# Optimization experiments

Hardware: AMD Instinct MI355X
Metric: run time of the kernel (lower is better)

Reference implementation:

```python
import jax, jax.numpy as jnp
import numpy as np

B, M, D, H = 32, 1024, 768, 256


def setup_inputs() -> dict:
    key = jax.random.key(0)
    k = jax.random.split(key, 6)
    V = jax.random.normal(k[0], (B, M, D), dtype=jnp.float32)
    alpha = jnp.float32(0.5)
    # torch nn.Linear weights: [out, in]
    WV_w = jax.random.normal(k[1], (H, D), dtype=jnp.float32) * (1.0 / np.sqrt(D))
    WV_b = jnp.zeros((H,), dtype=jnp.float32)
    W_conv = jax.random.normal(k[2], (H, H), dtype=jnp.float32) * (1.0 / np.sqrt(H))
    res_w = jax.random.normal(k[3], (H, D), dtype=jnp.float32) * (1.0 / np.sqrt(D))
    res_b = jnp.zeros((H,), dtype=jnp.float32)
    return {"V": V, "alpha": alpha, "WV_w": WV_w, "WV_b": WV_b,
            "W_conv": W_conv, "res_w": res_w, "res_b": res_b}


def reference(V, alpha, WV_w, WV_b, W_conv, res_w, res_b):
    # global feature awareness enhancement: alpha*V + (1-alpha)*mean
    g = jnp.mean(V, axis=1, keepdims=True)            # [B,1,D]
    V_enh = alpha * V + (1.0 - alpha) * g             # [B,M,D]
    # projection (torch Linear: x @ W.T + b)
    Vp = jnp.einsum('bmd,hd->bmh', V_enh, WV_w) + WV_b  # [B,M,H]
    # dynamic incidence matrix: row-softmax of Vp @ Vp.T
    sim = jnp.einsum('bmh,bnh->bmn', Vp, Vp)          # [B,M,M]
    H_TV = jax.nn.softmax(sim, axis=-1)               # [B,M,M]
    # hypergraph convolution: H @ ((H.T @ X) @ W)
    t1 = jnp.einsum('bnm,bnh->bmh', H_TV, Vp)         # H.T @ X -> [B,M,H]
    t2 = jnp.einsum('bmh,hk->bmk', t1, W_conv)        # [B,M,H]
    O = jnp.einsum('bmn,bnh->bmh', H_TV, t2)          # [B,M,H]
    # residual projection + relu
    res = jnp.einsum('bmd,hd->bmh', V, res_w) + res_b  # [B,M,H]
    return jax.nn.relu(O + res)
```

## Files before the change

### kernel.cpp

```cpp
#include <hip/hip_runtime.h>
#include <math.h>


#define PADK 40

typedef __attribute__((ext_vector_type(8))) short bf16x8;
typedef __attribute__((ext_vector_type(4))) float f32x4;

__device__ __forceinline__ ushort f2b(float f) {
    unsigned u = __float_as_uint(f);
    return (ushort)((u + 0x7fffu + ((u >> 16) & 1u)) >> 16);
}
__device__ __forceinline__ float b2f(ushort u) {
    return __uint_as_float((unsigned)u << 16);
}
__device__ __forceinline__ uint4 pack8(float4 a, float4 b) {
    uint4 r;
    r.x = f2b(a.x) | ((unsigned)f2b(a.y) << 16);
    r.y = f2b(a.z) | ((unsigned)f2b(a.w) << 16);
    r.z = f2b(b.x) | ((unsigned)f2b(b.y) << 16);
    r.w = f2b(b.z) | ((unsigned)f2b(b.w) << 16);
    return r;
}

template<bool CASTA>
__device__ __forceinline__ void gemm_core(const void* __restrict__ Av, int lda,
                                          const ushort* __restrict__ Bt, int ldb, int K,
                                          ushort* As, ushort* Bs, f32x4 acc[4][4]) {
    const int tid = threadIdx.x;
    const int lane = tid & 63;
    const int r0 = tid >> 2;
    const int c0 = (tid & 3) * 8;
    const int kg = (lane >> 4) * 8;
    const int rr = lane & 15;
    const int wave = tid >> 6;
    const int wr = (wave >> 1) * 64, wc = (wave & 1) * 64;
    ushort* as0 = As + r0 * PADK + c0;
    ushort* as1 = As + (r0 + 64) * PADK + c0;
    ushort* bs0 = Bs + r0 * PADK + c0;
    ushort* bs1 = Bs + (r0 + 64) * PADK + c0;
    const ushort* bt0 = Bt + (size_t)r0 * ldb + c0;
    const ushort* bt1 = Bt + (size_t)(r0 + 64) * ldb + c0;

    for (int k0 = 0; k0 < K; k0 += 32) {
        uint4 aw0, aw1;
        if constexpr (CASTA) {
            const float* fA = (const float*)Av;
            const float* pa0 = fA + (size_t)r0 * lda + k0 + c0;
            const float* pa1 = fA + (size_t)(r0 + 64) * lda + k0 + c0;
            aw0 = pack8(*(const float4*)pa0, *(const float4*)(pa0 + 4));
            aw1 = pack8(*(const float4*)pa1, *(const float4*)(pa1 + 4));
        } else {
            const ushort* uA = (const ushort*)Av;
            aw0 = *(const uint4*)(uA + (size_t)r0 * lda + k0 + c0);
            aw1 = *(const uint4*)(uA + (size_t)(r0 + 64) * lda + k0 + c0);
        }
        uint4 bw0 = *(const uint4*)(bt0 + k0);
        uint4 bw1 = *(const uint4*)(bt1 + k0);
        __syncthreads();
        *(uint4*)as0 = aw0; *(uint4*)as1 = aw1;
        *(uint4*)bs0 = bw0; *(uint4*)bs1 = bw1;
        __syncthreads();
        bf16x8 av[4], bv[4];
        #pragma unroll
        for (int i = 0; i < 4; ++i) {
            av[i] = *(const bf16x8*)(As + (wr + i * 16 + rr) * PADK + kg);
            bv[i] = *(const bf16x8*)(Bs + (wc + i * 16 + rr) * PADK + kg);
        }
        #pragma unroll
        for (int i = 0; i < 4; ++i)
            #pragma unroll
            for (int j = 0; j < 4; ++j)
                acc[i][j] = __builtin_amdgcn_mfma_f32_16x16x32_bf16(av[i], bv[j], acc[i][j], 0, 0, 0);
    }
}

#define EPI_COORDS \
    const int lane = threadIdx.x & 63; \
    const int wave = threadIdx.x >> 6; \
    const int rb = (wave >> 1) * 64 + (lane >> 4) * 4; \
    const int cb = (wave & 1) * 64 + (lane & 15);

__global__ __launch_bounds__(256) void k_mean(const float* __restrict__ V, float* __restrict__ gpart) {
    const int b = blockIdx.z, mc = blockIdx.y;
    const int d = blockIdx.x * 256 + threadIdx.x;
    const float* Vb = V + ((size_t)(b * 1024 + mc * 128)) * 768 + d;
    float s = 0.f;
    for (int m = 0; m < 128; ++m) s += Vb[(size_t)m * 768];
    gpart[(size_t)(mc * 32 + b) * 768 + d] = s;
}

__global__ __launch_bounds__(256) void k_gsum(const float* __restrict__ gpart, float* __restrict__ g) {
    int idx = blockIdx.x * 256 + threadIdx.x;
    float s = 0.f;
    #pragma unroll
    for (int c = 0; c < 8; ++c) s += gpart[(size_t)c * 24576 + idx];
    g[idx] = s * (1.0f / 1024.0f);
}

__global__ __launch_bounds__(256) void k_gW(const float* __restrict__ g,
                                            const float* __restrict__ WVw,
                                            float* __restrict__ gW) {
    int idx = blockIdx.x * 256 + threadIdx.x;
    int b = idx >> 8, h = idx & 255;
    const float* gr = g + b * 768;
    const float* wr = WVw + (size_t)h * 768;
    float s = 0.f;
    for (int d = 0; d < 768; ++d) s += gr[d] * wr[d];
    gW[idx] = s;
}

__global__ __launch_bounds__(256) void k_castw(const float* __restrict__ WVw,
                                               const float* __restrict__ resw,
                                               ushort* __restrict__ Wcat) {
    int id = blockIdx.x * 256 + threadIdx.x;
    int n = id / 96, c = (id - n * 96) * 8;
    const float* src = (n < 256) ? (WVw + (size_t)n * 768 + c) : (resw + (size_t)(n - 256) * 768 + c);
    *(uint4*)(Wcat + (size_t)n * 768 + c) = pack8(*(const float4*)src, *(const float4*)(src + 4));
}

__global__ __launch_bounds__(256) void k_wct(const float* __restrict__ Wc, ushort* __restrict__ WcT) {
    __shared__ float t[64][65];
    const int r0 = blockIdx.y * 64, c0 = blockIdx.x * 64;
    const int tid = threadIdx.x;
    #pragma unroll
    for (int i = 0; i < 4; ++i) {
        int r = (tid >> 4) + i * 16, c4 = (tid & 15) * 4;
        float4 v = *(const float4*)&Wc[(size_t)(r0 + r) * 256 + c0 + c4];
        t[r][c4] = v.x; t[r][c4 + 1] = v.y; t[r][c4 + 2] = v.z; t[r][c4 + 3] = v.w;
    }
    __syncthreads();
    #pragma unroll
    for (int i = 0; i < 4; ++i) {
        int oc = (tid >> 4) + i * 16, r4 = (tid & 15) * 4;
        unsigned lo = f2b(t[r4][oc]) | ((unsigned)f2b(t[r4 + 1][oc]) << 16);
        unsigned hi = f2b(t[r4 + 2][oc]) | ((unsigned)f2b(t[r4 + 3][oc]) << 16);
        *(uint2*)&WcT[(size_t)(c0 + oc) * 256 + r0 + r4] = make_uint2(lo, hi);
    }
}

__global__ __launch_bounds__(256) void k_trb(const ushort* __restrict__ in, ushort* __restrict__ out,
                                             int R, int C, int ldin) {
    __shared__ ushort t[64][68];
    const int b = blockIdx.z;
    const ushort* ib = in + (size_t)b * R * ldin;
    ushort* ob = out + (size_t)b * R * C;
    const int c0 = blockIdx.x * 64, r0 = blockIdx.y * 64;
    const int tid = threadIdx.x;
    #pragma unroll
    for (int i = 0; i < 4; ++i) {
        int r = (tid >> 4) + i * 16, c4 = (tid & 15) * 4;
        *(uint2*)&t[r][c4] = *(const uint2*)(ib + (size_t)(r0 + r) * ldin + c0 + c4);
    }
    __syncthreads();
    #pragma unroll
    for (int i = 0; i < 4; ++i) {
        int oc = (tid >> 4) + i * 16, r4 = (tid & 15) * 4;
        unsigned lo = t[r4][oc] | ((unsigned)t[r4 + 1][oc] << 16);
        unsigned hi = t[r4 + 2][oc] | ((unsigned)t[r4 + 3][oc] << 16);
        *(uint2*)(ob + (size_t)(c0 + oc) * R + r0 + r4) = make_uint2(lo, hi);
    }
}

__global__ __launch_bounds__(256) void k_proj(const float* __restrict__ V, const ushort* __restrict__ Wcat,
                                              const float* __restrict__ WVb, const float* __restrict__ resb,
                                              const float* __restrict__ gW, const float* __restrict__ alpha_p,
                                              ushort* __restrict__ Vp, ushort* __restrict__ resv) {
    __shared__ ushort As[128 * PADK], Bs[128 * PADK];
    f32x4 acc[4][4] = {};
    const int n0 = blockIdx.x * 128, m0 = blockIdx.y * 128;
    gemm_core<true>(V + (size_t)m0 * 768, 768, Wcat + (size_t)n0 * 768, 768, 768, As, Bs, acc);
    EPI_COORDS
    const float alpha = *alpha_p, oma = 1.0f - alpha;
    #pragma unroll
    for (int i = 0; i < 4; ++i)
        #pragma unroll
        for (int j = 0; j < 4; ++j) {
            int gcol = n0 + cb + j * 16;
            #pragma unroll
            for (int r = 0; r < 4; ++r) {
                int grow = m0 + rb + i * 16 + r;
                float v = acc[i][j][r];
                if (gcol < 256) {
                    float o = alpha * v + oma * gW[((grow >> 10) << 8) + gcol] + WVb[gcol];
                    Vp[(size_t)grow * 256 + gcol] = f2b(o);
                } else {
                    resv[(size_t)grow * 256 + gcol - 256] = f2b(v + resb[gcol - 256]);
                }
            }
        }
}

__global__ __launch_bounds__(256) void k_sim(const ushort* __restrict__ Vp, ushort* __restrict__ S) {
    __shared__ ushort As[128 * PADK], Bs[128 * PADK];
    f32x4 acc[4][4] = {};
    const int b = blockIdx.z;
    const ushort* Vb = Vp + (size_t)b * 1024 * 256;
    const int n0 = blockIdx.x * 128, m0 = blockIdx.y * 128;
    gemm_core<false>(Vb + (size_t)m0 * 256, 256, Vb + (size_t)n0 * 256, 256, 256, As, Bs, acc);
    ushort* Sb = S + ((size_t)b << 20);
    EPI_COORDS
    #pragma unroll
    for (int i = 0; i < 4; ++i)
        #pragma unroll
        for (int j = 0; j < 4; ++j)
            #pragma unroll
            for (int r = 0; r < 4; ++r)
                Sb[(size_t)(m0 + rb + i * 16 + r) * 1024 + n0 + cb + j * 16] = f2b(acc[i][j][r]);
}

__global__ __launch_bounds__(256) void k_softmax(ushort* __restrict__ S) {
    ushort* p = S + (size_t)blockIdx.x * 1024;
    const int tid = threadIdx.x;
    uint2 raw = *(const uint2*)(p + tid * 4);
    float f0 = b2f((ushort)(raw.x & 0xffff));
    float f1 = b2f((ushort)(raw.x >> 16));
    float f2 = b2f((ushort)(raw.y & 0xffff));
    float f3 = b2f((ushort)(raw.y >> 16));
    float lm = fmaxf(fmaxf(f0, f1), fmaxf(f2, f3));
    #pragma unroll
    for (int o = 32; o > 0; o >>= 1) lm = fmaxf(lm, __shfl_xor(lm, o, 64));
    __shared__ float red[4];
    const int wid = tid >> 6, lane = tid & 63;
    if (lane == 0) red[wid] = lm;
    __syncthreads();
    const float m = fmaxf(fmaxf(red[0], red[1]), fmaxf(red[2], red[3]));
    __syncthreads();
    f0 = __expf(f0 - m); f1 = __expf(f1 - m); f2 = __expf(f2 - m); f3 = __expf(f3 - m);
    float ls = f0 + f1 + f2 + f3;
    #pragma unroll
    for (int o = 32; o > 0; o >>= 1) ls += __shfl_xor(ls, o, 64);
    if (lane == 0) red[wid] = ls;
    __syncthreads();
    const float inv = 1.0f / (red[0] + red[1] + red[2] + red[3]);
    unsigned lo = f2b(f0 * inv) | ((unsigned)f2b(f1 * inv) << 16);
    unsigned hi = f2b(f2 * inv) | ((unsigned)f2b(f3 * inv) << 16);
    *(uint2*)(p + tid * 4) = make_uint2(lo, hi);
}

__global__ __launch_bounds__(256) void k_t1(const ushort* __restrict__ Pt, const ushort* __restrict__ VpT,
                                            ushort* __restrict__ t1) {
    __shared__ ushort As[128 * PADK], Bs[128 * PADK];
    f32x4 acc[4][4] = {};
    const int b = blockIdx.z;
    const int n0 = blockIdx.x * 128, m0 = blockIdx.y * 128;
    gemm_core<false>(Pt + ((size_t)b << 20) + (size_t)m0 * 1024, 1024,
                     VpT + (size_t)b * 256 * 1024 + (size_t)n0 * 1024, 1024, 1024, As, Bs, acc);
    ushort* ob = t1 + (size_t)b * 1024 * 256;
    EPI_COORDS
    #pragma unroll
    for (int i = 0; i < 4; ++i)
        #pragma unroll
        for (int j = 0; j < 4; ++j)
            #pragma unroll
            for (int r = 0; r < 4; ++r)
                ob[(size_t)(m0 + rb + i * 16 + r) * 256 + n0 + cb + j * 16] = f2b(acc[i][j][r]);
}

__global__ __launch_bounds__(256) void k_t2(const ushort* __restrict__ t1, const ushort* __restrict__ WcT,
                                            ushort* __restrict__ t2) {
    __shared__ ushort As[128 * PADK], Bs[128 * PADK];
    f32x4 acc[4][4] = {};
    const int n0 = blockIdx.x * 128, m0 = blockIdx.y * 128;
    gemm_core<false>(t1 + (size_t)m0 * 256, 256, WcT + (size_t)n0 * 256, 256, 256, As, Bs, acc);
    EPI_COORDS
    #pragma unroll
    for (int i = 0; i < 4; ++i)
        #pragma unroll
        for (int j = 0; j < 4; ++j)
            #pragma unroll
            for (int r = 0; r < 4; ++r)
                t2[(size_t)(m0 + rb + i * 16 + r) * 256 + n0 + cb + j * 16] = f2b(acc[i][j][r]);
}

__global__ __launch_bounds__(256) void k_O(const ushort* __restrict__ P, const ushort* __restrict__ t2T,
                                           const ushort* __restrict__ resv, float* __restrict__ out) {
    __shared__ ushort As[128 * PADK], Bs[128 * PADK];
    f32x4 acc[4][4] = {};
    const int b = blockIdx.z;
    const int n0 = blockIdx.x * 128, m0 = blockIdx.y * 128;
    gemm_core<false>(P + ((size_t)b << 20) + (size_t)m0 * 1024, 1024,
                     t2T + (size_t)b * 256 * 1024 + (size_t)n0 * 1024, 1024, 1024, As, Bs, acc);
    EPI_COORDS
    #pragma unroll
    for (int i = 0; i < 4; ++i)
        #pragma unroll
        for (int j = 0; j < 4; ++j)
            #pragma unroll
            for (int r = 0; r < 4; ++r) {
                size_t off = ((size_t)(b * 1024 + m0 + rb + i * 16 + r)) * 256 + n0 + cb + j * 16;
                out[off] = fmaxf(acc[i][j][r] + b2f(resv[off]), 0.0f);
            }
}

extern "C" void kernel_launch(void* const* d_in, const int* in_sizes, int n_in,
                              void* d_out, int out_size, void* d_ws, size_t ws_size,
                              hipStream_t stream) {
    const float* V     = (const float*)d_in[0];
    const float* alpha = (const float*)d_in[1];
    const float* WVw   = (const float*)d_in[2];
    const float* WVb   = (const float*)d_in[3];
    const float* Wc    = (const float*)d_in[4];
    const float* resw  = (const float*)d_in[5];
    const float* resb  = (const float*)d_in[6];
    float* out = (float*)d_out;

    char* W = (char*)d_ws;
    ushort* S    = (ushort*)(W);
    ushort* Vp   = (ushort*)(W + (64ull << 20));
    ushort* Pt   = (ushort*)(W + (64ull << 20));
    ushort* VpT  = (ushort*)(W + (128ull << 20));
    ushort* resv = (ushort*)(W + (144ull << 20));
    ushort* t1   = (ushort*)(W + (160ull << 20));
    ushort* WcT  = (ushort*)(W + (176ull << 20));
    ushort* Wcat = (ushort*)(W + (177ull << 20));
    float*  gpart= (float*)(W + (178ull << 20));
    float*  g    = (float*)(W + (179ull << 20));
    float*  gW   = (float*)(W + (179ull << 20) + (128u << 10));
    ushort* t2   = VpT;
    ushort* t2T  = t1;

    k_mean<<<dim3(3, 8, 32), 256, 0, stream>>>(V, gpart);
    k_gsum<<<96, 256, 0, stream>>>(gpart, g);
    k_gW<<<32, 256, 0, stream>>>(g, WVw, gW);
    k_castw<<<192, 256, 0, stream>>>(WVw, resw, Wcat);
    k_wct<<<dim3(4, 4), 256, 0, stream>>>(Wc, WcT);
    k_proj<<<dim3(4, 256), 256, 0, stream>>>(V, Wcat, WVb, resb, gW, alpha, Vp, resv);
    k_sim<<<dim3(8, 8, 32), 256, 0, stream>>>(Vp, S);
    k_trb<<<dim3(4, 16, 32), 256, 0, stream>>>(Vp, VpT, 1024, 256, 256);
    k_softmax<<<32768, 256, 0, stream>>>(S);
    k_trb<<<dim3(16, 16, 32), 256, 0, stream>>>(S, Pt, 1024, 1024, 1024);
    k_t1<<<dim3(2, 8, 32), 256, 0, stream>>>(Pt, VpT, t1);
    k_t2<<<dim3(2, 256), 256, 0, stream>>>(t1, WcT, t2);
    k_trb<<<dim3(4, 16, 32), 256, 0, stream>>>(t2, t2T, 1024, 256, 256);
    k_O<<<dim3(2, 8, 32), 256, 0, stream>>>(S, t2T, resv, out);
}
```

Baseline: 475.9 us.

## Exploit symmetric similarity with per-batch exp shift and async LDS GEMM loads

The row softmax is replaced by exp(sim - shift), where the shift is a per-batch maximum squared row norm. The result E is symmetric, so the 1024x1024 transpose and the separate softmax pass are dropped. Row normalisation moves into the transposed Vp operand for t1 and into the O epilogue via invZ. The GEMM core now uses global_load_lds with an XOR-swizzled 64-wide K tile, and V is cast to bf16 while the mean is computed. The risk is exp underflow for rows whose norm is far below the batch maximum.

```diff
diff --git a/kernel.cpp b/kernel.cpp
--- a/kernel.cpp
+++ b/kernel.cpp
@@ -1,8 +1,6 @@
 #include <hip/hip_runtime.h>
 #include <math.h>
 
-
-#define PADK 40
 
 typedef __attribute__((ext_vector_type(8))) short bf16x8;
 typedef __attribute__((ext_vector_type(4))) float f32x4;
@@ -23,55 +21,65 @@
     return r;
 }
 
-template<bool CASTA>
-__device__ __forceinline__ void gemm_core(const void* __restrict__ Av, int lda,
-                                          const ushort* __restrict__ Bt, int ldb, int K,
-                                          ushort* As, ushort* Bs, f32x4 acc[4][4]) {
+__device__ __forceinline__ void gl16(const void* g, void* l) {
+    __builtin_amdgcn_global_load_lds(
+        (__attribute__((address_space(1))) const unsigned*)g,
+        (__attribute__((address_space(3))) unsigned*)l, 16, 0, 0);
+}
+
+__device__ __forceinline__ void gemm_core(const ushort* __restrict__ A,
+                                          const ushort* __restrict__ Bt,
+                                          int K, ushort* As, ushort* Bs,
+                                          f32x4 acc[4][4]) {
     const int tid = threadIdx.x;
     const int lane = tid & 63;
-    const int r0 = tid >> 2;
-    const int c0 = (tid & 3) * 8;
-    const int kg = (lane >> 4) * 8;
+    const int wave = tid >> 6;
+    const int l8 = lane >> 3, l7 = lane & 7;
+    const int swz = ((l7 ^ l8) << 4);
+    const char* pa[4];
+    const char* pb[4];
+    ushort* la[4];
+    ushort* lb[4];
+    #pragma unroll
+    for (int i = 0; i < 4; ++i) {
+        int r = (wave * 4 + i) * 8 + l8;
+        pa[i] = (const char*)A + (size_t)r * (K * 2) + swz;
+        pb[i] = (const char*)Bt + (size_t)r * (K * 2) + swz;
+        la[i] = As + (wave * 4 + i) * 512;
+        lb[i] = Bs + (wave * 4 + i) * 512;
+    }
     const int rr = lane & 15;
-    const int wave = tid >> 6;
+    const int kq = (lane >> 4) << 4;
+    const int mask = (rr & 7) << 4;
+    const int c0 = kq ^ mask;
+    const int c1 = (64 + kq) ^ mask;
     const int wr = (wave >> 1) * 64, wc = (wave & 1) * 64;
-    ushort* as0 = As + r0 * PADK + c0;
-    ushort* as1 = As + (r0 + 64) * PADK + c0;
-    ushort* bs0 = Bs + r0 * PADK + c0;
-    ushort* bs1 = Bs + (r0 + 64) * PADK + c0;
-    const ushort* bt0 = Bt + (size_t)r0 * ldb + c0;
-    const ushort* bt1 = Bt + (size_t)(r0 + 64) * ldb + c0;
-
-    for (int k0 = 0; k0 < K; k0 += 32) {
-        uint4 aw0, aw1;
-        if constexpr (CASTA) {
-            const float* fA = (const float*)Av;
-            const float* pa0 = fA + (size_t)r0 * lda + k0 + c0;
-            const float* pa1 = fA + (size_t)(r0 + 64) * lda + k0 + c0;
-            aw0 = pack8(*(const float4*)pa0, *(const float4*)(pa0 + 4));
-            aw1 = pack8(*(const float4*)pa1, *(const float4*)(pa1 + 4));
-        } else {
-            const ushort* uA = (const ushort*)Av;
-            aw0 = *(const uint4*)(uA + (size_t)r0 * lda + k0 + c0);
-            aw1 = *(const uint4*)(uA + (size_t)(r0 + 64) * lda + k0 + c0);
+    const int arow0 = (wr + rr) * 128, brow0 = (wc + rr) * 128;
+
+    for (int k0 = 0; k0 < K; k0 += 64) {
+        __syncthreads();
+        #pragma unroll
+        for (int i = 0; i < 4; ++i) {
+            gl16(pa[i], la[i]);
+            gl16(pb[i], lb[i]);
+            pa[i] += 128; pb[i] += 128;
         }
-        uint4 bw0 = *(const uint4*)(bt0 + k0);
-        uint4 bw1 = *(const uint4*)(bt1 + k0);
         __syncthreads();
-        *(uint4*)as0 = aw0; *(uint4*)as1 = aw1;
-        *(uint4*)bs0 = bw0; *(uint4*)bs1 = bw1;
-        __syncthreads();
-        bf16x8 av[4], bv[4];
-        #pragma unroll
-        for (int i = 0; i < 4; ++i) {
-            av[i] = *(const bf16x8*)(As + (wr + i * 16 + rr) * PADK + kg);
-            bv[i] = *(const bf16x8*)(Bs + (wc + i * 16 + rr) * PADK + kg);
+        #pragma unroll
+        for (int ks = 0; ks < 2; ++ks) {
+            const int cc = ks ? c1 : c0;
+            bf16x8 av[4], bv[4];
+            #pragma unroll
+            for (int i = 0; i < 4; ++i) {
+                av[i] = *(const bf16x8*)((const char*)As + arow0 + i * 2048 + cc);
+                bv[i] = *(const bf16x8*)((const char*)Bs + brow0 + i * 2048 + cc);
+            }
+            #pragma unroll
+            for (int i = 0; i < 4; ++i)
+                #pragma unroll
+                for (int j = 0; j < 4; ++j)
+                    acc[i][j] = __builtin_amdgcn_mfma_f32_16x16x32_bf16(av[i], bv[j], acc[i][j], 0, 0, 0);
         }
-        #pragma unroll
-        for (int i = 0; i < 4; ++i)
-            #pragma unroll
-            for (int j = 0; j < 4; ++j)
-                acc[i][j] = __builtin_amdgcn_mfma_f32_16x16x32_bf16(av[i], bv[j], acc[i][j], 0, 0, 0);
     }
 }
 
@@ -81,13 +89,22 @@
     const int rb = (wave >> 1) * 64 + (lane >> 4) * 4; \
     const int cb = (wave & 1) * 64 + (lane & 15);
 
-__global__ __launch_bounds__(256) void k_mean(const float* __restrict__ V, float* __restrict__ gpart) {
-    const int b = blockIdx.z, mc = blockIdx.y;
-    const int d = blockIdx.x * 256 + threadIdx.x;
-    const float* Vb = V + ((size_t)(b * 1024 + mc * 128)) * 768 + d;
-    float s = 0.f;
-    for (int m = 0; m < 128; ++m) s += Vb[(size_t)m * 768];
-    gpart[(size_t)(mc * 32 + b) * 768 + d] = s;
+__global__ __launch_bounds__(192) void k_castmean(const float* __restrict__ V,
+                                                  ushort* __restrict__ Vb,
+                                                  float* __restrict__ gpart) {
+    const int b = blockIdx.x, mc = blockIdx.y, t = threadIdx.x;
+    const size_t base = ((size_t)(b * 1024 + mc * 128)) * 768 + t * 4;
+    const float* src = V + base;
+    ushort* dst = Vb + base;
+    float4 s = make_float4(0.f, 0.f, 0.f, 0.f);
+    for (int r = 0; r < 128; ++r) {
+        float4 v = *(const float4*)(src + (size_t)r * 768);
+        s.x += v.x; s.y += v.y; s.z += v.z; s.w += v.w;
+        unsigned u0 = f2b(v.x) | ((unsigned)f2b(v.y) << 16);
+        unsigned u1 = f2b(v.z) | ((unsigned)f2b(v.w) << 16);
+        *(uint2*)(dst + (size_t)r * 768) = make_uint2(u0, u1);
+    }
+    *(float4*)&gpart[(size_t)(mc * 32 + b) * 768 + t * 4] = s;
 }
 
 __global__ __launch_bounds__(256) void k_gsum(const float* __restrict__ gpart, float* __restrict__ g) {
@@ -139,37 +156,14 @@
     }
 }
 
-__global__ __launch_bounds__(256) void k_trb(const ushort* __restrict__ in, ushort* __restrict__ out,
-                                             int R, int C, int ldin) {
-    __shared__ ushort t[64][68];
-    const int b = blockIdx.z;
-    const ushort* ib = in + (size_t)b * R * ldin;
-    ushort* ob = out + (size_t)b * R * C;
-    const int c0 = blockIdx.x * 64, r0 = blockIdx.y * 64;
-    const int tid = threadIdx.x;
-    #pragma unroll
-    for (int i = 0; i < 4; ++i) {
-        int r = (tid >> 4) + i * 16, c4 = (tid & 15) * 4;
-        *(uint2*)&t[r][c4] = *(const uint2*)(ib + (size_t)(r0 + r) * ldin + c0 + c4);
-    }
-    __syncthreads();
-    #pragma unroll
-    for (int i = 0; i < 4; ++i) {
-        int oc = (tid >> 4) + i * 16, r4 = (tid & 15) * 4;
-        unsigned lo = t[r4][oc] | ((unsigned)t[r4 + 1][oc] << 16);
-        unsigned hi = t[r4 + 2][oc] | ((unsigned)t[r4 + 3][oc] << 16);
-        *(uint2*)(ob + (size_t)(c0 + oc) * R + r0 + r4) = make_uint2(lo, hi);
-    }
-}
-
-__global__ __launch_bounds__(256) void k_proj(const float* __restrict__ V, const ushort* __restrict__ Wcat,
+__global__ __launch_bounds__(256) void k_proj(const ushort* __restrict__ Vb, const ushort* __restrict__ Wcat,
                                               const float* __restrict__ WVb, const float* __restrict__ resb,
                                               const float* __restrict__ gW, const float* __restrict__ alpha_p,
                                               ushort* __restrict__ Vp, ushort* __restrict__ resv) {
-    __shared__ ushort As[128 * PADK], Bs[128 * PADK];
+    __shared__ ushort As[128 * 64], Bs[128 * 64];
     f32x4 acc[4][4] = {};
     const int n0 = blockIdx.x * 128, m0 = blockIdx.y * 128;
-    gemm_core<true>(V + (size_t)m0 * 768, 768, Wcat + (size_t)n0 * 768, 768, 768, As, Bs, acc);
+    gemm_core(Vb + (size_t)m0 * 768, Wcat + (size_t)n0 * 768, 768, As, Bs, acc);
     EPI_COORDS
     const float alpha = *alpha_p, oma = 1.0f - alpha;
     #pragma unroll
@@ -191,14 +185,39 @@
         }
 }
 
-__global__ __launch_bounds__(256) void k_sim(const ushort* __restrict__ Vp, ushort* __restrict__ S) {
-    __shared__ ushort As[128 * PADK], Bs[128 * PADK];
+__global__ __launch_bounds__(256) void k_dmax(const ushort* __restrict__ Vp, float* __restrict__ shift) {
+    const int b = blockIdx.x;
+    const int wave = threadIdx.x >> 6, lane = threadIdx.x & 63;
+    const ushort* Vb_ = Vp + (size_t)b * 1024 * 256;
+    float mx = -1e30f;
+    for (int rr = 0; rr < 256; ++rr) {
+        int row = wave * 256 + rr;
+        uint2 v = *(const uint2*)(Vb_ + (size_t)row * 256 + lane * 4);
+        float f0 = b2f((ushort)(v.x & 0xffff)), f1 = b2f((ushort)(v.x >> 16));
+        float f2 = b2f((ushort)(v.y & 0xffff)), f3 = b2f((ushort)(v.y >> 16));
+        float s = f0 * f0 + f1 * f1 + f2 * f2 + f3 * f3;
+        #pragma unroll
+        for (int o = 32; o > 0; o >>= 1) s += __shfl_xor(s, o, 64);
+        mx = fmaxf(mx, s);
+    }
+    __shared__ float red[4];
+    if (lane == 0) red[wave] = mx;
+    __syncthreads();
+    if (threadIdx.x == 0)
+        shift[b] = fmaxf(fmaxf(red[0], red[1]), fmaxf(red[2], red[3]));
+}
+
+__global__ __launch_bounds__(256) void k_sim(const ushort* __restrict__ Vp,
+                                             const float* __restrict__ shift,
+                                             ushort* __restrict__ E) {
+    __shared__ ushort As[128 * 64], Bs[128 * 64];
     f32x4 acc[4][4] = {};
     const int b = blockIdx.z;
-    const ushort* Vb = Vp + (size_t)b * 1024 * 256;
+    const ushort* Vb_ = Vp + (size_t)b * 1024 * 256;
     const int n0 = blockIdx.x * 128, m0 = blockIdx.y * 128;
-    gemm_core<false>(Vb + (size_t)m0 * 256, 256, Vb + (size_t)n0 * 256, 256, 256, As, Bs, acc);
-    ushort* Sb = S + ((size_t)b << 20);
+    gemm_core(Vb_ + (size_t)m0 * 256, Vb_ + (size_t)n0 * 256, 256, As, Bs, acc);
+    ushort* Eb = E + ((size_t)b << 20);
+    const float sh = shift[b];
     EPI_COORDS
     #pragma unroll
     for (int i = 0; i < 4; ++i)
@@ -206,46 +225,86 @@
         for (int j = 0; j < 4; ++j)
             #pragma unroll
             for (int r = 0; r < 4; ++r)
-                Sb[(size_t)(m0 + rb + i * 16 + r) * 1024 + n0 + cb + j * 16] = f2b(acc[i][j][r]);
-}
-
-__global__ __launch_bounds__(256) void k_softmax(ushort* __restrict__ S) {
-    ushort* p = S + (size_t)blockIdx.x * 1024;
+                Eb[(size_t)(m0 + rb + i * 16 + r) * 1024 + n0 + cb + j * 16] =
+                    f2b(__expf(acc[i][j][r] - sh));
+}
+
+__global__ __launch_bounds__(256) void k_rowsum(const ushort* __restrict__ E, float* __restrict__ invZ) {
+    const int row = blockIdx.x * 4 + (threadIdx.x >> 6);
+    const int lane = threadIdx.x & 63;
+    const ushort* p = E + (size_t)row * 1024 + lane * 4;
+    float s = 0.f;
+    #pragma unroll
+    for (int pass = 0; pass < 4; ++pass) {
+        uint2 v = *(const uint2*)(p + pass * 256);
+        s += b2f((ushort)(v.x & 0xffff)) + b2f((ushort)(v.x >> 16))
+           + b2f((ushort)(v.y & 0xffff)) + b2f((ushort)(v.y >> 16));
+    }
+    #pragma unroll
+    for (int o = 32; o > 0; o >>= 1) s += __shfl_xor(s, o, 64);
+    if (lane == 0) invZ[row] = 1.0f / s;
+}
+
+__global__ __launch_bounds__(256) void k_trbs(const ushort* __restrict__ Vp,
+                                              const float* __restrict__ invZ,
+                                              ushort* __restrict__ VpZT) {
+    __shared__ ushort t[64][68];
+    const int b = blockIdx.z;
+    const ushort* ib = Vp + (size_t)b * 1024 * 256;
+    ushort* ob = VpZT + (size_t)b * 256 * 1024;
+    const int c0 = blockIdx.x * 64, r0 = blockIdx.y * 64;
     const int tid = threadIdx.x;
-    uint2 raw = *(const uint2*)(p + tid * 4);
-    float f0 = b2f((ushort)(raw.x & 0xffff));
-    float f1 = b2f((ushort)(raw.x >> 16));
-    float f2 = b2f((ushort)(raw.y & 0xffff));
-    float f3 = b2f((ushort)(raw.y >> 16));
-    float lm = fmaxf(fmaxf(f0, f1), fmaxf(f2, f3));
-    #pragma unroll
-    for (int o = 32; o > 0; o >>= 1) lm = fmaxf(lm, __shfl_xor(lm, o, 64));
-    __shared__ float red[4];
-    const int wid = tid >> 6, lane = tid & 63;
-    if (lane == 0) red[wid] = lm;
+    #pragma unroll
+    for (int i = 0; i < 4; ++i) {
+        int r = (tid >> 4) + i * 16, c4 = (tid & 15) * 4;
+        uint2 v = *(const uint2*)(ib + (size_t)(r0 + r) * 256 + c0 + c4);
+        float iz = invZ[b * 1024 + r0 + r];
+        unsigned lo = f2b(b2f((ushort)(v.x & 0xffff)) * iz) |
+                      ((unsigned)f2b(b2f((ushort)(v.x >> 16)) * iz) << 16);
+        unsigned hi = f2b(b2f((ushort)(v.y & 0xffff)) * iz) |
+                      ((unsigned)f2b(b2f((ushort)(v.y >> 16)) * iz) << 16);
+        *(uint2*)&t[r][c4] = make_uint2(lo, hi);
+    }
     __syncthreads();
-    const float m = fmaxf(fmaxf(red[0], red[1]), fmaxf(red[2], red[3]));
+    #pragma unroll
+    for (int i = 0; i < 4; ++i) {
+        int oc = (tid >> 4) + i * 16, r4 = (tid & 15) * 4;
+        unsigned lo = t[r4][oc] | ((unsigned)t[r4 + 1][oc] << 16);
+        unsigned hi = t[r4 + 2][oc] | ((unsigned)t[r4 + 3][oc] << 16);
+        *(uint2*)(ob + (size_t)(c0 + oc) * 1024 + r0 + r4) = make_uint2(lo, hi);
+    }
+}
+
+__global__ __launch_bounds__(256) void k_trb(const ushort* __restrict__ in, ushort* __restrict__ out) {
+    __shared__ ushort t[64][68];
+    const int b = blockIdx.z;
+    const ushort* ib = in + (size_t)b * 1024 * 256;
+    ushort* ob = out + (size_t)b * 256 * 1024;
+    const int c0 = blockIdx.x * 64, r0 = blockIdx.y * 64;
+    const int tid = threadIdx.x;
+    #pragma unroll
+    for (int i = 0; i < 4; ++i) {
+        int r = (tid >> 4) + i * 16, c4 = (tid & 15) * 4;
+        *(uint2*)&t[r][c4] = *(const uint2*)(ib + (size_t)(r0 + r) * 256 + c0 + c4);
+    }
     __syncthreads();
-    f0 = __expf(f0 - m); f1 = __expf(f1 - m); f2 = __expf(f2 - m); f3 = __expf(f3 - m);
-    float ls = f0 + f1 + f2 + f3;
-    #pragma unroll
-    for (int o = 32; o > 0; o >>= 1) ls += __shfl_xor(ls, o, 64);
-    if (lane == 0) red[wid] = ls;
-    __syncthreads();
-    const float inv = 1.0f / (red[0] + red[1] + red[2] + red[3]);
-    unsigned lo = f2b(f0 * inv) | ((unsigned)f2b(f1 * inv) << 16);
-    unsigned hi = f2b(f2 * inv) | ((unsigned)f2b(f3 * inv) << 16);
-    *(uint2*)(p + tid * 4) = make_uint2(lo, hi);
-}
-
-__global__ __launch_bounds__(256) void k_t1(const ushort* __restrict__ Pt, const ushort* __restrict__ VpT,
+    #pragma unroll
+    for (int i = 0; i < 4; ++i) {
+        int oc = (tid >> 4) + i * 16, r4 = (tid & 15) * 4;
+        unsigned lo = t[r4][oc] | ((unsigned)t[r4 + 1][oc] << 16);
+        unsigned hi = t[r4 + 2][oc] | ((unsigned)t[r4 + 3][oc] << 16);
+        *(uint2*)(ob + (size_t)(c0 + oc) * 1024 + r0 + r4) = make_uint2(lo, hi);
+    }
+}
+
+__global__ __launch_bounds__(256) void k_t1(const ushort* __restrict__ E, const ushort* __restrict__ VpZT,
                                             ushort* __restrict__ t1) {
-    __shared__ ushort As[128 * PADK], Bs[128 * PADK];
+    __shared__ ushort As[128 * 64], Bs[128 * 64];
     f32x4 acc[4][4] = {};
     const int b = blockIdx.z;
     const int n0 = blockIdx.x * 128, m0 = blockIdx.y * 128;
-    gemm_core<false>(Pt + ((size_t)b << 20) + (size_t)m0 * 1024, 1024,
-                     VpT + (size_t)b * 256 * 1024 + (size_t)n0 * 1024, 1024, 1024, As, Bs, acc);
+    gemm_core(E + ((size_t)b << 20) + (size_t)m0 * 1024,
+              VpZT + (size_t)b * 256 * 1024 + (size_t)n0 * 1024, 1024, As, Bs, acc);
     ushort* ob = t1 + (size_t)b * 1024 * 256;
     EPI_COORDS
     #pragma unroll
@@ -259,10 +318,10 @@
 
 __global__ __launch_bounds__(256) void k_t2(const ushort* __restrict__ t1, const ushort* __restrict__ WcT,
                                             ushort* __restrict__ t2) {
-    __shared__ ushort As[128 * PADK], Bs[128 * PADK];
+    __shared__ ushort As[128 * 64], Bs[128 * 64];
     f32x4 acc[4][4] = {};
     const int n0 = blockIdx.x * 128, m0 = blockIdx.y * 128;
-    gemm_core<false>(t1 + (size_t)m0 * 256, 256, WcT + (size_t)n0 * 256, 256, 256, As, Bs, acc);
+    gemm_core(t1 + (size_t)m0 * 256, WcT + (size_t)n0 * 256, 256, As, Bs, acc);
     EPI_COORDS
     #pragma unroll
     for (int i = 0; i < 4; ++i)
@@ -273,14 +332,15 @@
                 t2[(size_t)(m0 + rb + i * 16 + r) * 256 + n0 + cb + j * 16] = f2b(acc[i][j][r]);
 }
 
-__global__ __launch_bounds__(256) void k_O(const ushort* __restrict__ P, const ushort* __restrict__ t2T,
-                                           const ushort* __restrict__ resv, float* __restrict__ out) {
-    __shared__ ushort As[128 * PADK], Bs[128 * PADK];
+__global__ __launch_bounds__(256) void k_O(const ushort* __restrict__ E, const ushort* __restrict__ t2T,
+                                           const ushort* __restrict__ resv, const float* __restrict__ invZ,
+                                           float* __restrict__ out) {
+    __shared__ ushort As[128 * 64], Bs[128 * 64];
     f32x4 acc[4][4] = {};
     const int b = blockIdx.z;
     const int n0 = blockIdx.x * 128, m0 = blockIdx.y * 128;
-    gemm_core<false>(P + ((size_t)b << 20) + (size_t)m0 * 1024, 1024,
-                     t2T + (size_t)b * 256 * 1024 + (size_t)n0 * 1024, 1024, 1024, As, Bs, acc);
+    gemm_core(E + ((size_t)b << 20) + (size_t)m0 * 1024,
+              t2T + (size_t)b * 256 * 1024 + (size_t)n0 * 1024, 1024, As, Bs, acc);
     EPI_COORDS
     #pragma unroll
     for (int i = 0; i < 4; ++i)
@@ -288,8 +348,10 @@
         for (int j = 0; j < 4; ++j)
             #pragma unroll
             for (int r = 0; r < 4; ++r) {
-                size_t off = ((size_t)(b * 1024 + m0 + rb + i * 16 + r)) * 256 + n0 + cb + j * 16;
-                out[off] = fmaxf(acc[i][j][r] + b2f(resv[off]), 0.0f);
+                int row = m0 + rb + i * 16 + r;
+                float iz = invZ[b * 1024 + row];
+                size_t off = ((size_t)(b * 1024 + row)) * 256 + n0 + cb + j * 16;
+                out[off] = fmaxf(acc[i][j][r] * iz + b2f(resv[off]), 0.0f);
             }
 }
 
@@ -306,32 +368,34 @@
     float* out = (float*)d_out;
 
     char* W = (char*)d_ws;
-    ushort* S    = (ushort*)(W);
-    ushort* Vp   = (ushort*)(W + (64ull << 20));
-    ushort* Pt   = (ushort*)(W + (64ull << 20));
-    ushort* VpT  = (ushort*)(W + (128ull << 20));
-    ushort* resv = (ushort*)(W + (144ull << 20));
+    ushort* Vb   = (ushort*)(W);
+    ushort* E    = (ushort*)(W + (48ull  << 20));
+    ushort* Vp   = (ushort*)(W + (112ull << 20));
+    ushort* resv = (ushort*)(W + (128ull << 20));
+    ushort* VpZT = (ushort*)(W + (144ull << 20));
     ushort* t1   = (ushort*)(W + (160ull << 20));
-    ushort* WcT  = (ushort*)(W + (176ull << 20));
-    ushort* Wcat = (ushort*)(W + (177ull << 20));
-    float*  gpart= (float*)(W + (178ull << 20));
-    float*  g    = (float*)(W + (179ull << 20));
-    float*  gW   = (float*)(W + (179ull << 20) + (128u << 10));
-    ushort* t2   = VpT;
-    ushort* t2T  = t1;
-
-    k_mean<<<dim3(3, 8, 32), 256, 0, stream>>>(V, gpart);
+    ushort* t2   = (ushort*)(W + (176ull << 20));
+    ushort* t2T  = (ushort*)(W + (192ull << 20));
+    ushort* Wcat = (ushort*)(W + (208ull << 20));
+    ushort* WcT  = (ushort*)(W + (209ull << 20));
+    float*  gpart= (float*) (W + (210ull << 20));
+    float*  g    = (float*) (W + (211ull << 20));
+    float*  gW   = (float*) (W + (211ull << 20) + (128u << 10));
+    float*  shv  = (float*) (W + (211ull << 20) + (256u << 10));
+    float*  invZ = (float*) (W + (212ull << 20));
+
+    k_castmean<<<dim3(32, 8), 192, 0, stream>>>(V, Vb, gpart);
     k_gsum<<<96, 256, 0, stream>>>(gpart, g);
     k_gW<<<32, 256, 0, stream>>>(g, WVw, gW);
     k_castw<<<192, 256, 0, stream>>>(WVw, resw, Wcat);
     k_wct<<<dim3(4, 4), 256, 0, stream>>>(Wc, WcT);
-    k_proj<<<dim3(4, 256), 256, 0, stream>>>(V, Wcat, WVb, resb, gW, alpha, Vp, resv);
-    k_sim<<<dim3(8, 8, 32), 256, 0, stream>>>(Vp, S);
-    k_trb<<<dim3(4, 16, 32), 256, 0, stream>>>(Vp, VpT, 1024, 256, 256);
-    k_softmax<<<32768, 256, 0, stream>>>(S);
-    k_trb<<<dim3(16, 16, 32), 256, 0, stream>>>(S, Pt, 1024, 1024, 1024);
-    k_t1<<<dim3(2, 8, 32), 256, 0, stream>>>(Pt, VpT, t1);
+    k_proj<<<dim3(4, 256), 256, 0, stream>>>(Vb, Wcat, WVb, resb, gW, alpha, Vp, resv);
+    k_dmax<<<32, 256, 0, stream>>>(Vp, shv);
+    k_sim<<<dim3(8, 8, 32), 256, 0, stream>>>(Vp, shv, E);
+    k_rowsum<<<8192, 256, 0, stream>>>(E, invZ);
+    k_trbs<<<dim3(4, 16, 32), 256, 0, stream>>>(Vp, invZ, VpZT);
+    k_t1<<<dim3(2, 8, 32), 256, 0, stream>>>(E, VpZT, t1);
     k_t2<<<dim3(2, 256), 256, 0, stream>>>(t1, WcT, t2);
-    k_trb<<<dim3(4, 16, 32), 256, 0, stream>>>(t2, t2T, 1024, 256, 256);
-    k_O<<<dim3(2, 8, 32), 256, 0, stream>>>(S, t2T, resv, out);
-}
+    k_trb<<<dim3(4, 16, 32), 256, 0, stream>>>(t2, t2T);
+    k_O<<<dim3(2, 8, 32), 256, 0, stream>>>(E, t2T, resv, invZ, out);
+}
```

Measured after the change: 469.4 us. Within noise of the previous version (-1.4%).
